# Performance work log

Measured on AMD Instinct MI355X. Metric: run time of the kernel, lower is better.

Reference implementation:

```python
import jax, jax.numpy as jnp
import numpy as np
from jax import lax


def squash(vec):
    # vec: [..., caps, dim]; squash along last dim (dim=2 in original layout [B, caps, dim])
    lensq = jnp.sum(vec * vec, axis=2)
    length = jnp.sqrt(lensq)
    scale = (lensq / (1.0 + lensq) / length)[:, :, None]
    return vec * scale


def setup_inputs() -> dict:
    key = jax.random.key(0)
    ks = jax.random.split(key, 6)
    stdv = 1.0 / np.sqrt(1152.0)
    return {
        "x": jax.random.normal(ks[0], (512, 1, 28, 28), dtype=jnp.float32),
        "conv1_w": jax.random.normal(ks[1], (256, 1, 9, 9), dtype=jnp.float32) * 0.05,
        "conv1_b": jax.random.normal(ks[2], (256,), dtype=jnp.float32) * 0.01,
        "conv2_w": jax.random.normal(ks[3], (256, 256, 9, 9), dtype=jnp.float32) * 0.01,
        "conv2_b": jax.random.normal(ks[4], (256,), dtype=jnp.float32) * 0.01,
        "caps_w": jax.random.uniform(ks[5], (1152, 8, 160), dtype=jnp.float32, minval=-stdv, maxval=stdv),
        "b_prior": jnp.zeros((1152, 10), dtype=jnp.float32),
    }


def reference(x, conv1_w, conv1_b, conv2_w, conv2_b, caps_w, b_prior):
    n_iterations = 3
    output_caps, output_dim = 10, 16
    dn = ("NCHW", "OIHW", "NCHW")

    # conv1 + relu: [N,1,28,28] -> [N,256,20,20]
    h = lax.conv_general_dilated(x, conv1_w, (1, 1), "VALID", dimension_numbers=dn)
    h = jax.nn.relu(h + conv1_b[None, :, None, None])

    # first capsule layer: conv k=9 s=2 -> [N,256,6,6]
    h = lax.conv_general_dilated(h, conv2_w, (2, 2), "VALID", dimension_numbers=dn)
    h = h + conv2_b[None, :, None, None]
    N, C, H, W = h.shape
    # [N, 32, 8, H, W] -> [N, 32, H, W, 8] -> [N, 32*H*W, 8]
    u = h.reshape(N, 32, 8, H, W).transpose(0, 1, 3, 4, 2).reshape(N, 32 * H * W, 8)
    u = squash(u)  # [N, 1152, 8]

    # prediction vectors: u_hat [N, 1152, 10, 16]
    u_hat = jnp.einsum("bid,ido->bio", u, caps_w).reshape(N, 1152, output_caps, output_dim)

    # dynamic routing-by-agreement
    c = jax.nn.softmax(b_prior, axis=1)  # [1152, 10]
    s = jnp.sum(c[None, :, :, None] * u_hat, axis=1)  # [N, 10, 16]
    v = squash(s)
    b_batch = jnp.broadcast_to(b_prior, (N, 1152, output_caps))
    for _ in range(n_iterations):
        b_batch = b_batch + jnp.sum(u_hat * v[:, None, :, :], axis=-1)  # agreement
        c = jax.nn.softmax(b_batch, axis=2)[..., None]  # [N, 1152, 10, 1]
        s = jnp.sum(c * u_hat, axis=1)
        v = squash(s)

    probs = jnp.sqrt(jnp.sum(v * v, axis=2))  # [N, 10]
    return (v, probs)
```

## Files before the change

kernel.cpp:

```cpp
#include <hip/hip_runtime.h>


#define N_IMG 512
#define RG 4

#define ARRS 12944
#define BUFS (4 * ARRS)
#define IMG_OFF (2 * BUFS)
#define W1L_OFF (IMG_OFF + 6272)
#define B1L_OFF (W1L_OFF + 10368)
#define SMEM_SZ (B1L_OFF + 128)

typedef __attribute__((ext_vector_type(8))) short bf16x8;
typedef __attribute__((ext_vector_type(4))) float f32x4;
typedef __attribute__((ext_vector_type(4))) unsigned int u32x4;

__device__ __forceinline__ unsigned short f2bf(float v) {
  unsigned int uu = __float_as_uint(v);
  uu += 0x7FFF + ((uu >> 16) & 1);
  return (unsigned short)(uu >> 16);
}
__device__ __forceinline__ float bf2f(unsigned short h) {
  return __uint_as_float(((unsigned int)h) << 16);
}
__device__ __forceinline__ int swz16(int row) {
  return (row ^ ((row >> 3) & 7)) << 4;
}

__global__ __launch_bounds__(256) void repack_b_kernel(
    const float* __restrict__ w2, unsigned short* __restrict__ bph,
    unsigned short* __restrict__ bpl) {
  __shared__ float slab[82 * 16 * 17];
  const int n = blockIdx.x, c = blockIdx.y;
  const int tid = threadIdx.x;
  for (int e = tid; e < 81 * 256; e += 256) {
    const int row = e / 81;
    const int rs = e - row * 81;
    const int co = row >> 4, ci = row & 15;
    slab[(rs * 16 + co) * 17 + ci] =
        w2[((size_t)(n * 16 + co) * 256 + c * 16 + ci) * 81 + rs];
  }
  __syncthreads();
  const int lane = tid & 63;
  const int l15 = lane & 15;
  const int lh = lane >> 5;
  const int cio8 = ((lane >> 4) & 1) * 8;
  for (int tt = tid >> 6; tt < 41; tt += 4) {
    const int rs = 2 * tt + lh;
    unsigned int hw[4], lw[4];
#pragma unroll
    for (int jp = 0; jp < 4; ++jp) {
      unsigned short h2[2], l2[2];
#pragma unroll
      for (int e = 0; e < 2; ++e) {
        const int j = jp * 2 + e;
        float v = (rs < 81) ? slab[(rs * 16 + l15) * 17 + cio8 + j] : 0.0f;
        unsigned short hh = f2bf(v);
        h2[e] = hh;
        l2[e] = f2bf(v - bf2f(hh));
      }
      hw[jp] = (unsigned int)h2[0] | ((unsigned int)h2[1] << 16);
      lw[jp] = (unsigned int)l2[0] | ((unsigned int)l2[1] << 16);
    }
    const size_t off = (((size_t)n * 656 + c * 41 + tt) * 64 + lane) * 8;
    *(u32x4*)(bph + off) = (u32x4){hw[0], hw[1], hw[2], hw[3]};
    *(u32x4*)(bpl + off) = (u32x4){lw[0], lw[1], lw[2], lw[3]};
  }
}

__global__ __launch_bounds__(160) void repack_cw_kernel(
    const float* __restrict__ cw, float* __restrict__ cwt) {
  __shared__ float t[8][160];
  const int i = blockIdx.x;
  const int od = threadIdx.x;
#pragma unroll
  for (int k = 0; k < 8; ++k) t[k][od] = cw[((size_t)i * 8 + k) * 160 + od];
  __syncthreads();
  float4 o0 = {t[0][od], t[1][od], t[2][od], t[3][od]};
  float4 o1 = {t[4][od], t[5][od], t[6][od], t[7][od]};
  float4* dst = (float4*)(cwt + ((size_t)i * 160 + od) * 8);
  dst[0] = o0;
  dst[1] = o1;
}

__global__ __launch_bounds__(256) void c0_kernel(const float* __restrict__ bp,
                                                 float* __restrict__ c0b) {
  const int i = blockIdx.x * 256 + threadIdx.x;
  if (i >= 1152) return;
  float b[10];
  float m = -1e30f;
#pragma unroll
  for (int o = 0; o < 10; ++o) {
    b[o] = bp[i * 10 + o];
    m = fmaxf(m, b[o]);
  }
  float sum = 0.0f;
#pragma unroll
  for (int o = 0; o < 10; ++o) {
    b[o] = __expf(b[o] - m);
    sum += b[o];
  }
  const float inv = 1.0f / sum;
#pragma unroll
  for (int o = 0; o < 10; ++o) c0b[i * 10 + o] = b[o] * inv;
}

__global__ __launch_bounds__(256) void gemm_s0_kernel(
    const float* __restrict__ u, const float* __restrict__ cw,
    const float* __restrict__ c0b, float* __restrict__ s0p) {
  __shared__ float a_l[64 * 257];
  __shared__ float b_l[64 * 160];
  __shared__ float c0_l[320];
  const int mt = blockIdx.x;
  const int ks = blockIdx.y;
  const int m0 = mt * 64;
  const int tid = threadIdx.x;
  const int mb = tid >> 4;
  const int ob = (tid & 15) * 10;

  for (int i = tid; i < 320; i += 256) c0_l[i] = c0b[(ks * 32) * 10 + i];
  for (int idx = tid; idx < 16384; idx += 256) {
    const int m = idx >> 8, kk = idx & 255;
    a_l[m * 257 + kk] = u[(size_t)(m0 + m) * 9216 + ks * 256 + kk];
  }

  float acc[4][10];
#pragma unroll
  for (int r = 0; r < 4; ++r)
#pragma unroll
    for (int c = 0; c < 10; ++c) acc[r][c] = 0.0f;

#pragma unroll 1
  for (int kc = 0; kc < 4; ++kc) {
    __syncthreads();
    for (int idx = tid; idx < 10240; idx += 256) {
      const int kk = idx / 160, od = idx - kk * 160;
      const int kg = kc * 64 + kk;
      b_l[kk * 160 + od] = cw[((size_t)ks * 256 + kg) * 160 + od] *
                           c0_l[(kg >> 3) * 10 + (od >> 4)];
    }
    __syncthreads();
#pragma unroll 4
    for (int kk = 0; kk < 64; ++kk) {
      float a4[4];
#pragma unroll
      for (int r = 0; r < 4; ++r)
        a4[r] = a_l[(mb * 4 + r) * 257 + kc * 64 + kk];
      const float* bp_ = &b_l[kk * 160 + ob];
#pragma unroll
      for (int c = 0; c < 10; ++c) {
        const float bv = bp_[c];
#pragma unroll
        for (int r = 0; r < 4; ++r) acc[r][c] = fmaf(a4[r], bv, acc[r][c]);
      }
    }
  }

#pragma unroll
  for (int r = 0; r < 4; ++r) {
#pragma unroll
    for (int c = 0; c < 10; ++c) {
      s0p[((size_t)ks * N_IMG + m0 + mb * 4 + r) * 160 + ob + c] = acc[r][c];
    }
  }
}

template <int H>
__device__ __forceinline__ void conv1_half(const float* __restrict__ ib,
                                           const float* __restrict__ w1l,
                                           char* __restrict__ abase, int ch,
                                           int oy, int ig, float bv1) {
  float a[10];
#pragma unroll
  for (int ox = 0; ox < 10; ++ox) a[ox] = bv1;
#pragma unroll
  for (int r = 0; r < 9; ++r) {
    float row[20];
    const float4* rp = (const float4*)&ib[(oy + r) * 28 + H * 8];
#pragma unroll
    for (int q = 0; q < 5; ++q) {
      float4 v4 = rp[q];
      row[4 * q + 0] = v4.x; row[4 * q + 1] = v4.y;
      row[4 * q + 2] = v4.z; row[4 * q + 3] = v4.w;
    }
#pragma unroll
    for (int s = 0; s < 9; ++s) {
      const float wval = w1l[ch * 81 + r * 9 + s];
#pragma unroll
      for (int ox = 0; ox < 10; ++ox)
        a[ox] = fmaf(row[ox + s + 2 * H], wval, a[ox]);
    }
  }
  const int arrA = (ch >> 3) * ARRS;
  const int colB = (ch & 7) * 2;
  const int rowBase = ig * 400 + oy * 20 + H * 10;
#pragma unroll
  for (int q = 0; q < 10; ++q) {
    const float v = fmaxf(a[q], 0.0f);
    const unsigned short hi = f2bf(v);
    const unsigned short lo = f2bf(v - bf2f(hi));
    const int sb = swz16(rowBase + q);
    *(unsigned short*)(abase + arrA + sb + colB) = hi;
    *(unsigned short*)(abase + 2 * ARRS + arrA + sb + colB) = lo;
  }
}

__global__ __launch_bounds__(512, 1) void fused_conv_kernel(
    const float* __restrict__ x, const float* __restrict__ w1,
    const float* __restrict__ b1, const unsigned short* __restrict__ bph,
    const unsigned short* __restrict__ bpl, const float* __restrict__ b2,
    float* __restrict__ u) {
  __shared__ __align__(16) char smem[SMEM_SZ];
  float* img = (float*)(smem + IMG_OFF);
  float* sq = (float*)smem;

  const int bp2 = blockIdx.x;
  const int tid = threadIdx.x;
  const int wid = tid >> 6;
  const int lane = tid & 63;
  const int l15 = lane & 15;
  const int lq4 = lane >> 4;
  const int lqb = lq4 & 1;
  const int lh = lane >> 5;
  const int g = wid & 3;

  int rowb[5];
  bool okm[5];
#pragma unroll
  for (int mt = 0; mt < 5; ++mt) {
    const int m = mt * 16 + l15;
    okm[mt] = (m < 72);
    const int mm = okm[mt] ? m : 0;
    const int im = (mm >= 36) ? 1 : 0;
    const int p = mm - 36 * im;
    const int oy = p / 6, ox = p - 6 * oy;
    rowb[mt] = im * 400 + 40 * oy + 2 * ox;
  }

  for (int i = tid; i < 1568; i += 512) img[i] = x[bp2 * 1568 + i];
  if (tid < 32) {
    *(int*)(smem + (tid >> 2) * ARRS + 804 * 16 + (tid & 3) * 4) = 0;
  }
  for (int i = tid; i < 1296; i += 512) ((float*)(smem + W1L_OFF))[i] = w1[i];
  if (tid < 16) ((float*)(smem + B1L_OFF))[tid] = b1[tid];
  __syncthreads();

  f32x4 acc[5][4];
#pragma unroll
  for (int mt = 0; mt < 5; ++mt)
#pragma unroll
    for (int nn = 0; nn < 4; ++nn) acc[mt][nn] = (f32x4){0.f, 0.f, 0.f, 0.f};

#define MFMA_STEP(CBH, CBL, J, DOPF)                                       \
  {                                                                        \
    const int rs_ = 2 * (J) + lh;                                          \
    const int r_ = (rs_ * 57) >> 9;                                        \
    const int s_ = rs_ - 9 * r_;                                           \
    const int rs20_ = 20 * r_ + s_;                                        \
    const bool okrs_ = (rs_ <= 80);                                        \
    bf16x8 ah[5], al[5];                                                   \
    _Pragma("unroll") for (int mt = 0; mt < 5; ++mt) {                     \
      const int row_ = (okm[mt] && okrs_) ? (rowb[mt] + rs20_) : 800;      \
      const int ad_ = swz16(row_);                                         \
      ah[mt] = *(const bf16x8*)(hbase + ad_);                              \
      al[mt] = *(const bf16x8*)(lbase + ad_);                              \
    }                                                                      \
    _Pragma("unroll") for (int mt = 0; mt < 5; ++mt) {                     \
      _Pragma("unroll") for (int nn = 0; nn < 4; ++nn) {                   \
        acc[mt][nn] = __builtin_amdgcn_mfma_f32_16x16x32_bf16(             \
            al[mt], CBH[nn], acc[mt][nn], 0, 0, 0);                        \
        acc[mt][nn] = __builtin_amdgcn_mfma_f32_16x16x32_bf16(             \
            ah[mt], CBL[nn], acc[mt][nn], 0, 0, 0);                        \
        acc[mt][nn] = __builtin_amdgcn_mfma_f32_16x16x32_bf16(             \
            ah[mt], CBH[nn], acc[mt][nn], 0, 0, 0);                        \
      }                                                                    \
    }                                                                      \
    if ((DOPF) && (J) + 2 < 41) {                                          \
      _Pragma("unroll") for (int nn = 0; nn < 4; ++nn) {                   \
        CBH[nn] = *(const bf16x8*)(pb[nn] + (size_t)((J) + 2) * 512);      \
        CBL[nn] = *(const bf16x8*)(pl[nn] + (size_t)((J) + 2) * 512);      \
      }                                                                    \
    }                                                                      \
  }

#pragma unroll 1
  for (int it = 0; it <= 16; ++it) {
    if (wid >= 4) {
      if (it < 16) {
        const float* w1l = (float*)(smem + W1L_OFF) + (it & 1) * 1296;
        const float* b1l = (float*)(smem + B1L_OFF) + (it & 1) * 16;
        char* abase = smem + (it & 1) * BUFS;
        for (int t = tid - 256; t < 1280; t += 256) {
          const int half = (t >= 640) ? 1 : 0;
          const int rest = t - half * 640;
          const int ig = rest / 320;
          const int r2 = rest - ig * 320;
          const int ch = r2 & 15;
          const int oy = r2 >> 4;
          const float* ib = &img[ig * 784];
          const float bv1 = b1l[ch];
          if (half == 0)
            conv1_half<0>(ib, w1l, abase, ch, oy, ig, bv1);
          else
            conv1_half<1>(ib, w1l, abase, ch, oy, ig, bv1);
        }
        if (it + 1 < 16) {
          float* w1n = (float*)(smem + W1L_OFF) + ((it + 1) & 1) * 1296;
          for (int i = tid - 256; i < 1296; i += 256)
            w1n[i] = w1[(it + 1) * 1296 + i];
          if (tid - 256 < 16)
            ((float*)(smem + B1L_OFF))[((it + 1) & 1) * 16 + (tid - 256)] =
                b1[(it + 1) * 16 + (tid - 256)];
        }
      }
    } else {
      if (it >= 1) {
        const int cc = it - 1;
        const unsigned short* pb[4];
        const unsigned short* pl[4];
#pragma unroll
        for (int nn = 0; nn < 4; ++nn) {
          const size_t base =
              ((size_t)(g * 4 + nn) * 656 + cc * 41) * 512 + lane * 8;
          pb[nn] = bph + base;
          pl[nn] = bpl + base;
        }
        bf16x8 cbh0[4], cbl0[4], cbh1[4], cbl1[4];
#pragma unroll
        for (int nn = 0; nn < 4; ++nn) {
          cbh0[nn] = *(const bf16x8*)(pb[nn]);
          cbl0[nn] = *(const bf16x8*)(pl[nn]);
          cbh1[nn] = *(const bf16x8*)(pb[nn] + 512);
          cbl1[nn] = *(const bf16x8*)(pl[nn] + 512);
        }
        const char* hbase = smem + (cc & 1) * BUFS + lqb * ARRS;
        const char* lbase = smem + (cc & 1) * BUFS + 2 * ARRS + lqb * ARRS;
        int j = 0;
#pragma unroll 1
        for (; j + 1 < 41; j += 2) {
          MFMA_STEP(cbh0, cbl0, j, 1);
          MFMA_STEP(cbh1, cbl1, j + 1, 1);
        }
        MFMA_STEP(cbh0, cbl0, 40, 0);
      }
    }
    __syncthreads();
  }
#undef MFMA_STEP

  if (wid < 4) {
    float b2v[4];
#pragma unroll
    for (int nn = 0; nn < 4; ++nn) b2v[nn] = b2[(g * 4 + nn) * 16 + l15];
#pragma unroll
    for (int mt = 0; mt < 5; ++mt) {
#pragma unroll
      for (int i = 0; i < 4; ++i) {
        const int m = mt * 16 + lq4 * 4 + i;
        if (m < 72) {
          const int im = (m >= 36) ? 1 : 0;
          const int p36 = m - 36 * im;
#pragma unroll
          for (int nn = 0; nn < 4; ++nn) {
            sq[(im * 256 + (g * 4 + nn) * 16 + l15) * 36 + p36] =
                acc[mt][nn][i] + b2v[nn];
          }
        }
      }
    }
  }
  __syncthreads();

  for (int i = tid; i < 2304; i += 512) {
    const int ig = i / 1152;
    const int cap = i - ig * 1152;
    const int gg = cap / 36, yx = cap - 36 * gg;
    float vals[8];
    float lensq = 0.0f;
#pragma unroll
    for (int d = 0; d < 8; ++d) {
      vals[d] = sq[(ig * 256 + gg * 8 + d) * 36 + yx];
      lensq = fmaf(vals[d], vals[d], lensq);
    }
    const float len = sqrtf(lensq);
    const float scale = lensq / (1.0f + lensq) / len;
    float4* dst = (float4*)(u + ((size_t)(bp2 * 2 + ig) * 1152 + cap) * 8);
    float4 lo4, hi4;
    lo4.x = vals[0] * scale; lo4.y = vals[1] * scale;
    lo4.z = vals[2] * scale; lo4.w = vals[3] * scale;
    hi4.x = vals[4] * scale; hi4.y = vals[5] * scale;
    hi4.z = vals[6] * scale; hi4.w = vals[7] * scale;
    dst[0] = lo4; dst[1] = hi4;
  }
}

__global__ __launch_bounds__(256) void routing_a_kernel(
    const float* __restrict__ u, const float* __restrict__ cwt,
    const float* __restrict__ b_prior, const float* __restrict__ vsum,
    float* __restrict__ s_part) {
  __shared__ float u_l[RG * 16 * 8];
  __shared__ float uhat[RG][16][161];
  __shared__ float v_l[RG * 160];
  __shared__ float bp_l[32 * 10];
  __shared__ float c_l[RG * 16 * 10];
  __shared__ float s_acc[RG * 160];

  const int gb = blockIdx.x;
  const int ch = blockIdx.y;
  const int cap0 = ch * 32;
  const int b0 = gb * RG;
  const int tid = threadIdx.x;

  for (int i = tid; i < RG * 160; i += 256) {
    const int g = i / 160, od = i - g * 160;
    v_l[i] = vsum[(b0 + g) * 160 + od];
    s_acc[i] = 0.0f;
  }
  for (int i = tid; i < 320; i += 256) bp_l[i] = b_prior[cap0 * 10 + i];

#pragma unroll 1
  for (int cc = 0; cc < 2; ++cc) {
    const int c16 = cap0 + cc * 16;
    __syncthreads();
    for (int i = tid; i < RG * 128; i += 256) {
      const int g = i >> 7, off = i & 127;
      u_l[g * 128 + off] = u[((size_t)(b0 + g) * 1152 + c16) * 8 + off];
    }
    __syncthreads();

    for (int e = tid; e < 2560; e += 256) {
      const int i = e / 160, od = e - i * 160;
      const float4* wp =
          (const float4*)(cwt + ((size_t)(c16 + i) * 160 + od) * 8);
      const float4 wa = wp[0], wb = wp[1];
#pragma unroll
      for (int g = 0; g < RG; ++g) {
        const float* up = &u_l[(g * 16 + i) * 8];
        float a = up[0] * wa.x;
        a = fmaf(up[1], wa.y, a);
        a = fmaf(up[2], wa.z, a);
        a = fmaf(up[3], wa.w, a);
        a = fmaf(up[4], wb.x, a);
        a = fmaf(up[5], wb.y, a);
        a = fmaf(up[6], wb.z, a);
        a = fmaf(up[7], wb.w, a);
        uhat[g][i][od] = a;
      }
    }
    __syncthreads();

    for (int e = tid; e < RG * 160; e += 256) {
      const int g = e / 160;
      const int r = e - g * 160;
      const int i = r / 10, o = r - i * 10;
      float agg = 0.0f;
#pragma unroll
      for (int d = 0; d < 16; ++d)
        agg = fmaf(uhat[g][i][o * 16 + d], v_l[g * 160 + o * 16 + d], agg);
      c_l[e] = bp_l[(cc * 16 + i) * 10 + o] + agg;
    }
    __syncthreads();

    if (tid < RG * 16) {
      const int g = tid >> 4, i = tid & 15;
      float bb[10];
      float m = -1e30f;
#pragma unroll
      for (int o = 0; o < 10; ++o) {
        bb[o] = c_l[(g * 16 + i) * 10 + o];
        m = fmaxf(m, bb[o]);
      }
      float sum = 0.0f;
#pragma unroll
      for (int o = 0; o < 10; ++o) {
        bb[o] = __expf(bb[o] - m);
        sum += bb[o];
      }
      const float inv = 1.0f / sum;
#pragma unroll
      for (int o = 0; o < 10; ++o) c_l[(g * 16 + i) * 10 + o] = bb[o] * inv;
    }
    __syncthreads();

    for (int e = tid; e < RG * 160; e += 256) {
      const int g = e / 160, od = e - g * 160;
      const int o = od >> 4;
      float a = 0.0f;
#pragma unroll
      for (int i = 0; i < 16; ++i)
        a = fmaf(c_l[(g * 16 + i) * 10 + o], uhat[g][i][od], a);
      s_acc[e] += a;
    }
  }
  __syncthreads();

  for (int e = tid; e < RG * 160; e += 256) {
    const int g = e / 160, od = e - g * 160;
    s_part[((size_t)ch * N_IMG + b0 + g) * 160 + od] = s_acc[e];
  }
}

__global__ __launch_bounds__(192) void routing_b_kernel(
    const float* __restrict__ s_part, int nchunk, float* __restrict__ v_out,
    float* __restrict__ probs, float* __restrict__ vsum, int mode) {
  __shared__ float s_l[160];
  __shared__ float scale_l[10];
  __shared__ float len_l[10];
  const int b = blockIdx.x;
  const int t = threadIdx.x;
  if (t < 160) {
    float a = 0.0f;
    for (int ch = 0; ch < nchunk; ++ch)
      a += s_part[((size_t)ch * N_IMG + b) * 160 + t];
    s_l[t] = a;
  }
  __syncthreads();
  if (t < 10) {
    float lensq = 0.0f;
#pragma unroll
    for (int d = 0; d < 16; ++d) {
      const float xv = s_l[t * 16 + d];
      lensq = fmaf(xv, xv, lensq);
    }
    const float len = sqrtf(lensq);
    scale_l[t] = lensq / (1.0f + lensq) / len;
    len_l[t] = lensq / (1.0f + lensq);
  }
  __syncthreads();
  if (t < 160) {
    const float vv = s_l[t] * scale_l[t / 16];
    v_out[b * 160 + t] = vv;
    if (mode == 0) vsum[b * 160 + t] = vv;
    else if (mode == 1) vsum[b * 160 + t] += vv;
  }
  if (t < 10) probs[b * 10 + t] = len_l[t];
}

extern "C" void kernel_launch(void* const* d_in, const int* in_sizes, int n_in,
                              void* d_out, int out_size, void* d_ws,
                              size_t ws_size, hipStream_t stream) {
  const float* x  = (const float*)d_in[0];
  const float* w1 = (const float*)d_in[1];
  const float* b1 = (const float*)d_in[2];
  const float* w2 = (const float*)d_in[3];
  const float* b2 = (const float*)d_in[4];
  const float* cw = (const float*)d_in[5];
  const float* bp = (const float*)d_in[6];

  float* out = (float*)d_out;
  float* v_out = out;
  float* probs = out + N_IMG * 160;

  float* base = (float*)d_ws;
  unsigned short* bph = (unsigned short*)d_ws;
  unsigned short* bpl = bph + (size_t)16 * 656 * 512;
  float* u    = base + 5373952;
  float* vsum = u + 4718592;
  float* c0b  = vsum + 81920;
  float* cwt = base;
  float* sp  = base + 1474560;

  repack_b_kernel<<<dim3(16, 16), 256, 0, stream>>>(w2, bph, bpl);
  fused_conv_kernel<<<256, 512, 0, stream>>>(x, w1, b1, bph, bpl, b2, u);
  c0_kernel<<<5, 256, 0, stream>>>(bp, c0b);
  repack_cw_kernel<<<1152, 160, 0, stream>>>(cw, cwt);
  gemm_s0_kernel<<<dim3(8, 36), 256, 0, stream>>>(u, cw, c0b, sp);
  routing_b_kernel<<<N_IMG, 192, 0, stream>>>(sp, 36, v_out, probs, vsum, 0);
  for (int pass = 1; pass < 4; ++pass) {
    const int mode = (pass < 3) ? 1 : 2;
    routing_a_kernel<<<dim3(N_IMG / RG, 36), 256, 0, stream>>>(u, cwt, bp,
                                                               vsum, sp);
    routing_b_kernel<<<N_IMG, 192, 0, stream>>>(sp, 36, v_out, probs, vsum,
                                                mode);
  }
}
```

Before: 1.158 ms.

## Drop warp-specialized double buffering for uniform waves and two blocks per CU

Replaces the producer/consumer split, where four waves ran conv1 into a double-buffered LDS tile while four waves ran MFMA, with a single-buffered scheme. All eight waves now compute conv1, synchronize, then all do MFMA, each on two output-channel tiles instead of four. Halving LDS use and accumulator registers allows two blocks per CU through launch bounds (512, 2). The cost is the loss of intra-block overlap between conv1 and MFMA, plus extra barriers per chunk, in exchange for overlap across co-resident blocks.

Measured after the change: 1.704 ms. 1.47x slower.

```diff
diff --git a/kernel.cpp b/kernel.cpp
--- a/kernel.cpp
+++ b/kernel.cpp
@@ -5,11 +5,11 @@
 #define RG 4
 
 #define ARRS 12944
-#define BUFS (4 * ARRS)
-#define IMG_OFF (2 * BUFS)
+#define A_SZ (4 * ARRS)
+#define IMG_OFF A_SZ
 #define W1L_OFF (IMG_OFF + 6272)
-#define B1L_OFF (W1L_OFF + 10368)
-#define SMEM_SZ (B1L_OFF + 128)
+#define B1L_OFF (W1L_OFF + 5184)
+#define SMEM_SZ 73728
 
 typedef __attribute__((ext_vector_type(8))) short bf16x8;
 typedef __attribute__((ext_vector_type(4))) float f32x4;
@@ -205,13 +205,15 @@
   }
 }
 
-__global__ __launch_bounds__(512, 1) void fused_conv_kernel(
+__global__ __launch_bounds__(512, 2) void fused_conv_kernel(
     const float* __restrict__ x, const float* __restrict__ w1,
     const float* __restrict__ b1, const unsigned short* __restrict__ bph,
     const unsigned short* __restrict__ bpl, const float* __restrict__ b2,
     float* __restrict__ u) {
   __shared__ __align__(16) char smem[SMEM_SZ];
   float* img = (float*)(smem + IMG_OFF);
+  float* w1l = (float*)(smem + W1L_OFF);
+  float* b1l = (float*)(smem + B1L_OFF);
   float* sq = (float*)smem;
 
   const int bp2 = blockIdx.x;
@@ -222,7 +224,6 @@
   const int lq4 = lane >> 4;
   const int lqb = lq4 & 1;
   const int lh = lane >> 5;
-  const int g = wid & 3;
 
   int rowb[5];
   bool okm[5];
@@ -238,18 +239,18 @@
   }
 
   for (int i = tid; i < 1568; i += 512) img[i] = x[bp2 * 1568 + i];
-  if (tid < 32) {
+  if (tid < 16) {
     *(int*)(smem + (tid >> 2) * ARRS + 804 * 16 + (tid & 3) * 4) = 0;
   }
-  for (int i = tid; i < 1296; i += 512) ((float*)(smem + W1L_OFF))[i] = w1[i];
-  if (tid < 16) ((float*)(smem + B1L_OFF))[tid] = b1[tid];
-  __syncthreads();
-
-  f32x4 acc[5][4];
+
+  f32x4 acc[5][2];
 #pragma unroll
   for (int mt = 0; mt < 5; ++mt)
 #pragma unroll
-    for (int nn = 0; nn < 4; ++nn) acc[mt][nn] = (f32x4){0.f, 0.f, 0.f, 0.f};
+    for (int nn = 0; nn < 2; ++nn) acc[mt][nn] = (f32x4){0.f, 0.f, 0.f, 0.f};
+
+  const char* hbase = smem + lqb * ARRS;
+  const char* lbase = smem + 2 * ARRS + lqb * ARRS;
 
 #define MFMA_STEP(CBH, CBL, J, DOPF)                                       \
   {                                                                        \
@@ -266,7 +267,7 @@
       al[mt] = *(const bf16x8*)(lbase + ad_);                              \
     }                                                                      \
     _Pragma("unroll") for (int mt = 0; mt < 5; ++mt) {                     \
-      _Pragma("unroll") for (int nn = 0; nn < 4; ++nn) {                   \
+      _Pragma("unroll") for (int nn = 0; nn < 2; ++nn) {                   \
         acc[mt][nn] = __builtin_amdgcn_mfma_f32_16x16x32_bf16(             \
             al[mt], CBH[nn], acc[mt][nn], 0, 0, 0);                        \
         acc[mt][nn] = __builtin_amdgcn_mfma_f32_16x16x32_bf16(             \
@@ -276,7 +277,7 @@
       }                                                                    \
     }                                                                      \
     if ((DOPF) && (J) + 2 < 41) {                                          \
-      _Pragma("unroll") for (int nn = 0; nn < 4; ++nn) {                   \
+      _Pragma("unroll") for (int nn = 0; nn < 2; ++nn) {                   \
         CBH[nn] = *(const bf16x8*)(pb[nn] + (size_t)((J) + 2) * 512);      \
         CBL[nn] = *(const bf16x8*)(pl[nn] + (size_t)((J) + 2) * 512);      \
       }                                                                    \
@@ -284,74 +285,61 @@
   }
 
 #pragma unroll 1
-  for (int it = 0; it <= 16; ++it) {
-    if (wid >= 4) {
-      if (it < 16) {
-        const float* w1l = (float*)(smem + W1L_OFF) + (it & 1) * 1296;
-        const float* b1l = (float*)(smem + B1L_OFF) + (it & 1) * 16;
-        char* abase = smem + (it & 1) * BUFS;
-        for (int t = tid - 256; t < 1280; t += 256) {
-          const int half = (t >= 640) ? 1 : 0;
-          const int rest = t - half * 640;
-          const int ig = rest / 320;
-          const int r2 = rest - ig * 320;
-          const int ch = r2 & 15;
-          const int oy = r2 >> 4;
-          const float* ib = &img[ig * 784];
-          const float bv1 = b1l[ch];
-          if (half == 0)
-            conv1_half<0>(ib, w1l, abase, ch, oy, ig, bv1);
-          else
-            conv1_half<1>(ib, w1l, abase, ch, oy, ig, bv1);
-        }
-        if (it + 1 < 16) {
-          float* w1n = (float*)(smem + W1L_OFF) + ((it + 1) & 1) * 1296;
-          for (int i = tid - 256; i < 1296; i += 256)
-            w1n[i] = w1[(it + 1) * 1296 + i];
-          if (tid - 256 < 16)
-            ((float*)(smem + B1L_OFF))[((it + 1) & 1) * 16 + (tid - 256)] =
-                b1[(it + 1) * 16 + (tid - 256)];
-        }
-      }
-    } else {
-      if (it >= 1) {
-        const int cc = it - 1;
-        const unsigned short* pb[4];
-        const unsigned short* pl[4];
-#pragma unroll
-        for (int nn = 0; nn < 4; ++nn) {
-          const size_t base =
-              ((size_t)(g * 4 + nn) * 656 + cc * 41) * 512 + lane * 8;
-          pb[nn] = bph + base;
-          pl[nn] = bpl + base;
-        }
-        bf16x8 cbh0[4], cbl0[4], cbh1[4], cbl1[4];
-#pragma unroll
-        for (int nn = 0; nn < 4; ++nn) {
-          cbh0[nn] = *(const bf16x8*)(pb[nn]);
-          cbl0[nn] = *(const bf16x8*)(pl[nn]);
-          cbh1[nn] = *(const bf16x8*)(pb[nn] + 512);
-          cbl1[nn] = *(const bf16x8*)(pl[nn] + 512);
-        }
-        const char* hbase = smem + (cc & 1) * BUFS + lqb * ARRS;
-        const char* lbase = smem + (cc & 1) * BUFS + 2 * ARRS + lqb * ARRS;
-        int j = 0;
+  for (int c = 0; c < 16; ++c) {
+    const unsigned short* pb[2];
+    const unsigned short* pl[2];
+#pragma unroll
+    for (int nn = 0; nn < 2; ++nn) {
+      const size_t base =
+          ((size_t)(wid * 2 + nn) * 656 + c * 41) * 512 + lane * 8;
+      pb[nn] = bph + base;
+      pl[nn] = bpl + base;
+    }
+    bf16x8 cbh0[2], cbl0[2], cbh1[2], cbl1[2];
+#pragma unroll
+    for (int nn = 0; nn < 2; ++nn) {
+      cbh0[nn] = *(const bf16x8*)(pb[nn]);
+      cbl0[nn] = *(const bf16x8*)(pl[nn]);
+      cbh1[nn] = *(const bf16x8*)(pb[nn] + 512);
+      cbl1[nn] = *(const bf16x8*)(pl[nn] + 512);
+    }
+
+    __syncthreads();
+    for (int i = tid; i < 1296; i += 512) w1l[i] = w1[c * 1296 + i];
+    if (tid < 16) b1l[tid] = b1[c * 16 + tid];
+    __syncthreads();
+
+    for (int t = tid; t < 1280; t += 512) {
+      const int half = (t >= 640) ? 1 : 0;
+      const int rest = t - half * 640;
+      const int ig = rest / 320;
+      const int r2 = rest - ig * 320;
+      const int ch = r2 & 15;
+      const int oy = r2 >> 4;
+      const float* ib = &img[ig * 784];
+      const float bv1 = b1l[ch];
+      if (half == 0)
+        conv1_half<0>(ib, w1l, smem, ch, oy, ig, bv1);
+      else
+        conv1_half<1>(ib, w1l, smem, ch, oy, ig, bv1);
+    }
+    __syncthreads();
+
+    int j = 0;
 #pragma unroll 1
-        for (; j + 1 < 41; j += 2) {
-          MFMA_STEP(cbh0, cbl0, j, 1);
-          MFMA_STEP(cbh1, cbl1, j + 1, 1);
-        }
-        MFMA_STEP(cbh0, cbl0, 40, 0);
-      }
-    }
-    __syncthreads();
+    for (; j + 1 < 41; j += 2) {
+      MFMA_STEP(cbh0, cbl0, j, 1);
+      MFMA_STEP(cbh1, cbl1, j + 1, 1);
+    }
+    MFMA_STEP(cbh0, cbl0, 40, 0);
   }
 #undef MFMA_STEP
 
-  if (wid < 4) {
-    float b2v[4];
-#pragma unroll
-    for (int nn = 0; nn < 4; ++nn) b2v[nn] = b2[(g * 4 + nn) * 16 + l15];
+  __syncthreads();
+  {
+    float b2v[2];
+#pragma unroll
+    for (int nn = 0; nn < 2; ++nn) b2v[nn] = b2[(wid * 2 + nn) * 16 + l15];
 #pragma unroll
     for (int mt = 0; mt < 5; ++mt) {
 #pragma unroll
@@ -361,8 +349,8 @@
           const int im = (m >= 36) ? 1 : 0;
           const int p36 = m - 36 * im;
 #pragma unroll
-          for (int nn = 0; nn < 4; ++nn) {
-            sq[(im * 256 + (g * 4 + nn) * 16 + l15) * 36 + p36] =
+          for (int nn = 0; nn < 2; ++nn) {
+            sq[(im * 256 + (wid * 2 + nn) * 16 + l15) * 36 + p36] =
                 acc[mt][nn][i] + b2v[nn];
           }
         }
```
